# Performance work log

Hardware: AMD Instinct MI355X
Metric: run time of the kernel (lower is better)

Reference implementation:

```python
import jax, jax.numpy as jnp
import numpy as np

DIM = 768
H = 6        # pinned by router mask construction (3 logits -> 6 head gates)
HD = DIM // H  # 128
TAU = 5.0

def setup_inputs() -> dict:
    key = jax.random.key(0)
    ks = jax.random.split(key, 10)
    w = 0.02
    return {
        "x": jax.random.normal(ks[0], (4, 2048, DIM), jnp.float32),
        "latency": jax.random.uniform(ks[1], (1,), jnp.float32),
        "qkv_w": jax.random.normal(ks[2], (3 * DIM, DIM), jnp.float32) * w,
        "qkv_b": jax.random.normal(ks[3], (3 * DIM,), jnp.float32) * w,
        "proj_w": jax.random.normal(ks[4], (DIM, DIM), jnp.float32) * w,
        "proj_b": jax.random.normal(ks[5], (DIM,), jnp.float32) * w,
        "router_w": jax.random.normal(ks[6], (3, 1), jnp.float32),
        "router_b": jax.random.normal(ks[7], (3,), jnp.float32),
        # gumbel noise g = -log(Exp(1)), matching -empty.exponential_().log()
        "g1": -jnp.log(jax.random.exponential(ks[8], (3,), jnp.float32)),
        "g2": -jnp.log(jax.random.exponential(ks[9], (3,), jnp.float32)),
    }

def reference(x, latency, qkv_w, qkv_b, proj_w, proj_b, router_w, router_b, g1, g2):
    # router: Linear(1, 3) on scalar latency -> 3 logits
    logits = router_w @ latency + router_b                      # [3]
    # gumbel-sigmoid, tau=5, hard=True with straight-through estimator
    y_soft = jax.nn.sigmoid((logits + g1 - g2) / TAU)           # [3]
    y_hard = (y_soft > 0.5).astype(y_soft.dtype)
    mask3 = y_hard - jax.lax.stop_gradient(y_soft) + y_soft     # [3]
    # first logit gates 4 heads, remaining two gate one head each -> 6 heads
    mask6 = jnp.concatenate([mask3[:1], mask3[:1], mask3[:1], mask3])  # [6]
    maskC = jnp.repeat(mask6, HD)                               # [DIM]

    B, N, C = x.shape
    qkv = jnp.einsum('bnc,oc->bno', x, qkv_w) + qkv_b           # [B,N,3*DIM]
    qkv = qkv.reshape(B, N, 3, H, HD)
    q, k, v = qkv[:, :, 0], qkv[:, :, 1], qkv[:, :, 2]          # [B,N,H,HD]

    scale = HD ** -0.5
    attn = jax.nn.softmax(jnp.einsum('bqhd,bkhd->bhqk', q * scale, k), axis=-1)
    out = jnp.einsum('bhqk,bkhd->bqhd', attn, v).reshape(B, N, C)

    out = out * maskC                                            # gate heads/channels
    return jnp.einsum('bnc,oc->bno', out, proj_w) + proj_b
```

## Files before the change

### kernel.cpp

```cpp
#include <hip/hip_runtime.h>
#include <cstdint>

#define DIM_ 768
#define H_ 6
#define HD_ 128
#define NB_ 4
#define SEQ_ 2048
#define TOK_ (NB_*SEQ_)
#define OUT3_ (3*DIM_)
#define L2E 1.4426950408889634f

typedef __bf16 bf16;
typedef __bf16 bf16x4 __attribute__((ext_vector_type(4)));
typedef __bf16 bf16x8 __attribute__((ext_vector_type(8)));
typedef float f32x4 __attribute__((ext_vector_type(4)));
typedef float f32x16 __attribute__((ext_vector_type(16)));
typedef unsigned int u32;
typedef u32 u32x4 __attribute__((ext_vector_type(4)));

__device__ __forceinline__ void gload16(const void* g, void* lds) {
  __builtin_amdgcn_global_load_lds((const __attribute__((address_space(1))) void*)g,
                                   (__attribute__((address_space(3))) void*)lds,
                                   16, 0, 0);
}

__global__ void convert_kernel(const float* __restrict__ in, bf16* __restrict__ out, int n) {
  int i = (blockIdx.x * 256 + threadIdx.x) * 4;
  if (i >= n) return;
  float4 v = *reinterpret_cast<const float4*>(in + i);
  bf16x4 o = { (bf16)v.x, (bf16)v.y, (bf16)v.z, (bf16)v.w };
  *reinterpret_cast<bf16x4*>(out + i) = o;
}

__global__ void mask_kernel(const float* __restrict__ latency,
                            const float* __restrict__ rw,
                            const float* __restrict__ rb,
                            const float* __restrict__ g1,
                            const float* __restrict__ g2,
                            float* __restrict__ mask6) {
  int i = threadIdx.x;
  if (i < 6) {
    int j = (i < 4) ? 0 : (i - 3);
    float logit = rw[j] * latency[0] + rb[j];
    float z = (logit + g1[j] - g2[j]) / 5.0f;
    float ys = 1.0f / (1.0f + expf(-z));
    float yh = ys > 0.5f ? 1.0f : 0.0f;
    mask6[i] = (yh - ys) + ys;
  }
}


__global__ __launch_bounds__(256)
void qkv_gemm(const bf16* __restrict__ A, const bf16* __restrict__ W,
              const float* __restrict__ bias,
              bf16* __restrict__ q, bf16* __restrict__ k, bf16* __restrict__ vt) {
  __shared__ bf16 As[128 * 32];
  __shared__ bf16 Bs[128 * 32];
  __shared__ bf16 FragS[8192];
  const int tid = threadIdx.x;
  const int l = tid & 63, w = tid >> 6;
  const int lr = l & 15, lg = l >> 4;
  const int wm = w >> 1, wn = w & 1;
  const int tm = blockIdx.y * 128;
  const int on = blockIdx.x * 128;

  f32x4 acc[4][4];
#pragma unroll
  for (int i = 0; i < 4; ++i)
#pragma unroll
    for (int j = 0; j < 4; ++j) acc[i][j] = f32x4{0.f, 0.f, 0.f, 0.f};

  for (int k0 = 0; k0 < DIM_; k0 += 32) {
    __syncthreads();
#pragma unroll
    for (int u = 0; u < 2; ++u) {
      int row = w * 32 + u * 16 + (l >> 2);
      int cb = l & 3;
      gload16(A + (size_t)(tm + row) * DIM_ + k0 + cb * 8, As + (w * 32 + u * 16) * 32);
      gload16(W + (size_t)(on + row) * DIM_ + k0 + cb * 8, Bs + (w * 32 + u * 16) * 32);
    }
    __syncthreads();
    bf16x8 af[4], bfr[4];
#pragma unroll
    for (int i = 0; i < 4; ++i)
      af[i] = *reinterpret_cast<const bf16x8*>(As + (wm * 64 + i * 16 + lr) * 32 + lg * 8);
#pragma unroll
    for (int j = 0; j < 4; ++j)
      bfr[j] = *reinterpret_cast<const bf16x8*>(Bs + (wn * 64 + j * 16 + lr) * 32 + lg * 8);
#pragma unroll
    for (int i = 0; i < 4; ++i)
#pragma unroll
      for (int j = 0; j < 4; ++j)
        acc[i][j] = __builtin_amdgcn_mfma_f32_16x16x32_bf16(af[i], bfr[j], acc[i][j], 0, 0, 0);
  }

  if (on < 2 * DIM_) {
    const int s = on / DIM_;
    const float scale = 0.08838834764831845f * L2E;
    const int n0 = tm & 2047;
    const int bb = tm >> 11;
    const int hh = (on - s * DIM_) >> 7;
    const int bhh = bb * H_ + hh;
    bf16* dstbase = (s == 0) ? q : k;
    for (int pass = 0; pass < 2; ++pass) {
      __syncthreads();
      if (wm == pass) {
#pragma unroll
        for (int i = 0; i < 4; ++i) {
#pragma unroll
          for (int j = 0; j < 4; ++j) {
            int dd = wn * 64 + j * 16 + lr;
            int kc = dd >> 4, hi8 = (dd >> 3) & 1, e = dd & 7;
            float bia = bias[on + dd];
#pragma unroll
            for (int r = 0; r < 4; ++r) {
              int nl = i * 16 + lg * 4 + r;
              float val = acc[i][j][r] + bia;
              if (s == 0) val *= scale;
              FragS[(((nl >> 5) * 8 + kc) << 9) + ((hi8 * 32 + (nl & 31)) << 3) + e] = (bf16)val;
            }
          }
        }
      }
      __syncthreads();
      size_t base = ((size_t)bhh * 64 + (n0 >> 5) + pass * 2) * 4096;
#pragma unroll
      for (int r8 = 0; r8 < 4; ++r8) {
        bf16x8 v8 = *reinterpret_cast<const bf16x8*>(FragS + r8 * 2048 + tid * 8);
        *reinterpret_cast<bf16x8*>(dstbase + base + r8 * 2048 + tid * 8) = v8;
      }
    }
  } else {
    const int hh = (on - 2 * DIM_) >> 7;
    const int bb = tm >> 11, n0 = tm & 2047;
    const int bhh = bb * H_ + hh;
    bf16(*Ts)[136] = reinterpret_cast<bf16(*)[136]>(As);
    for (int wc = 0; wc < 2; ++wc) {
#pragma unroll
      for (int j = 0; j < 4; ++j) {
        __syncthreads();
        if (wn == wc) {
          float bia = bias[on + wc * 64 + j * 16 + lr];
#pragma unroll
          for (int i = 0; i < 4; ++i) {
            bf16x4 pk;
#pragma unroll
            for (int r = 0; r < 4; ++r) pk[r] = (bf16)(acc[i][j][r] + bia);
            *reinterpret_cast<bf16x4*>(&Ts[lr][wm * 64 + i * 16 + lg * 4]) = pk;
          }
        }
        __syncthreads();
        int row = tid >> 4;
        int c8 = (tid & 15) * 8;
        bf16x8 v8 = *reinterpret_cast<const bf16x8*>(&Ts[row][c8]);
        int d = wc * 64 + j * 16 + row;
        int n = n0 + c8;
        size_t idx = (((((size_t)bhh * 32 + (n >> 6)) * 4 + ((n >> 4) & 3)) * 4 + (d >> 5)) << 9) +
                     ((((n >> 3) & 1) * 32 + (d & 31)) << 3);
        *reinterpret_cast<bf16x8*>(vt + idx) = v8;
      }
    }
  }
}

__global__ __launch_bounds__(256)
void proj_gemm(const bf16* __restrict__ A, const bf16* __restrict__ W,
               const float* __restrict__ bias, float* __restrict__ out) {
  __shared__ bf16 As[128 * 32];
  __shared__ bf16 Bs[128 * 32];
  const int tid = threadIdx.x;
  const int l = tid & 63, w = tid >> 6;
  const int lr = l & 15, lg = l >> 4;
  const int wm = w >> 1, wn = w & 1;
  const int tm = blockIdx.y * 128;
  const int on = blockIdx.x * 128;

  f32x4 acc[4][4];
#pragma unroll
  for (int i = 0; i < 4; ++i)
#pragma unroll
    for (int j = 0; j < 4; ++j) acc[i][j] = f32x4{0.f, 0.f, 0.f, 0.f};

  for (int k0 = 0; k0 < DIM_; k0 += 32) {
    __syncthreads();
#pragma unroll
    for (int u = 0; u < 2; ++u) {
      int row = w * 32 + u * 16 + (l >> 2);
      int cb = l & 3;
      gload16(A + (size_t)(tm + row) * DIM_ + k0 + cb * 8, As + (w * 32 + u * 16) * 32);
      gload16(W + (size_t)(on + row) * DIM_ + k0 + cb * 8, Bs + (w * 32 + u * 16) * 32);
    }
    __syncthreads();
    bf16x8 af[4], bfr[4];
#pragma unroll
    for (int i = 0; i < 4; ++i)
      af[i] = *reinterpret_cast<const bf16x8*>(As + (wm * 64 + i * 16 + lr) * 32 + lg * 8);
#pragma unroll
    for (int j = 0; j < 4; ++j)
      bfr[j] = *reinterpret_cast<const bf16x8*>(Bs + (wn * 64 + j * 16 + lr) * 32 + lg * 8);
#pragma unroll
    for (int i = 0; i < 4; ++i)
#pragma unroll
      for (int j = 0; j < 4; ++j)
        acc[i][j] = __builtin_amdgcn_mfma_f32_16x16x32_bf16(af[i], bfr[j], acc[i][j], 0, 0, 0);
  }

#pragma unroll
  for (int i = 0; i < 4; ++i) {
#pragma unroll
    for (int j = 0; j < 4; ++j) {
      int o = on + wn * 64 + j * 16 + lr;
      float bia = bias[o];
#pragma unroll
      for (int r = 0; r < 4; ++r) {
        int t = tm + wm * 64 + i * 16 + lg * 4 + r;
        out[(size_t)t * DIM_ + o] = acc[i][j][r] + bia;
      }
    }
  }
}

__global__ __launch_bounds__(256)
void attn_kernel(const bf16* __restrict__ qf_g, const bf16* __restrict__ kf_g,
                 const bf16* __restrict__ vf_g, const float* __restrict__ mask6,
                 bf16* __restrict__ ab) {
  __shared__ char smem[33280];

  const int tid = threadIdx.x;
  const int l = tid & 63;
  const int w = tid >> 6;
  const int half = w >> 1, qw = w & 1;
  const int kl = l & 31, hi = l >> 5;
  const int bid = blockIdx.x;
  const int bh = bid % 24;
  const int qt2 = bid / 24;
  const int h = bh % H_;
  const int b = bh / H_;
  const int q0 = qt2 * 64 + qw * 32;
  const int loff = l * 8;
  const float hm = mask6[h];

  if (hm == 0.0f) {
    bf16x8 z = __builtin_bit_cast(bf16x8, u32x4{0u, 0u, 0u, 0u});
    int row = tid >> 2, c0 = (tid & 3) * 32;
    bf16* dst = ab + ((size_t)b * SEQ_ + qt2 * 64 + row) * DIM_ + h * HD_ + c0;
#pragma unroll
    for (int u = 0; u < 4; ++u)
      *reinterpret_cast<bf16x8*>(dst + u * 8) = z;
    return;
  }

  bf16* KSh = (bf16*)(smem + half * 8192);
  bf16* VSh = (bf16*)(smem + 16384 + half * 8192);
  float* MLm = (float*)(smem + 32768);
  float* MLl = MLm + 64;

  const bf16* qq = qf_g + (((size_t)bh * 64 + qt2 * 2 + qw) * 8) * 512;
  const bf16* kq = kf_g + (size_t)bh * 262144;
  const bf16* vq = vf_g + (size_t)bh * 262144;

  bf16x8 qf[8];
#pragma unroll
  for (int kc = 0; kc < 8; ++kc)
    qf[kc] = *reinterpret_cast<const bf16x8*>(qq + kc * 512 + loff);

  f32x16 oacc[4];
#pragma unroll
  for (int df = 0; df < 4; ++df)
#pragma unroll
    for (int r = 0; r < 16; ++r) oacc[df][r] = 0.f;
  float m_lane = -3.0e38f;
  float lsum = 0.f;

  for (int it = 0; it < 32; ++it) {
    int jj = half * 32 + it;
#pragma unroll
    for (int u = 0; u < 4; ++u) {
      int c = qw * 4 + u;
      gload16(kq + (size_t)jj * 4096 + c * 512 + loff, KSh + c * 512);
      gload16(vq + (size_t)jj * 4096 + c * 512 + loff, VSh + c * 512);
    }
    __syncthreads();

    f32x16 sacc;
#pragma unroll
    for (int r = 0; r < 16; ++r) sacc[r] = 0.f;
    __builtin_amdgcn_s_setprio(1);
#pragma unroll
    for (int kc = 0; kc < 8; ++kc) {
      bf16x8 kfr = *reinterpret_cast<const bf16x8*>(KSh + kc * 512 + loff);
      sacc = __builtin_amdgcn_mfma_f32_32x32x16_bf16(kfr, qf[kc], sacc, 0, 0, 0);
    }
    __builtin_amdgcn_s_setprio(0);

    float t = sacc[0];
#pragma unroll
    for (int r = 1; r < 16; ++r) t = fmaxf(t, sacc[r]);
    t = fmaxf(t, __shfl_xor(t, 32));
    bool need = t > m_lane + 8.0f;
    if (__ballot(need) != 0ull) {
      float nm = fmaxf(m_lane, t);
      float c = exp2f(m_lane - nm);
      m_lane = nm;
      lsum *= c;
#pragma unroll
      for (int r = 0; r < 16; ++r) {
        float cr = __shfl(c, (r & 3) + 8 * (r >> 2) + 4 * hi);
#pragma unroll
        for (int df = 0; df < 4; ++df) oacc[df][r] *= cr;
      }
    }

    u32 pp[8];
#pragma unroll
    for (int m = 0; m < 8; ++m) {
      float e0 = exp2f(sacc[2 * m] - m_lane);
      float e1 = exp2f(sacc[2 * m + 1] - m_lane);
      lsum += e0 + e1;
      union { u32 u; bf16 hh2[2]; } pk;
      pk.hh2[0] = (bf16)e0; pk.hh2[1] = (bf16)e1;
      pp[m] = pk.u;
    }

    u32x4 afv[2];
#pragma unroll
    for (int ks = 0; ks < 2; ++ks) {
#pragma unroll
      for (int i = 0; i < 2; ++i) {
        u32 a = pp[4 * ks + i];
        u32 b2 = pp[4 * ks + 2 + i];
        asm volatile("v_permlane32_swap_b32 %0, %1" : "+v"(a), "+v"(b2));
        afv[ks][i] = a;
        afv[ks][2 + i] = b2;
      }
    }

    __builtin_amdgcn_s_setprio(1);
#pragma unroll
    for (int ks = 0; ks < 2; ++ks) {
      bf16x8 pa = __builtin_bit_cast(bf16x8, afv[ks]);
#pragma unroll
      for (int df = 0; df < 4; ++df) {
        bf16x8 vfr = *reinterpret_cast<const bf16x8*>(VSh + (ks * 4 + df) * 512 + loff);
        oacc[df] = __builtin_amdgcn_mfma_f32_32x32x16_bf16(pa, vfr, oacc[df], 0, 0, 0);
      }
    }
    __builtin_amdgcn_s_setprio(0);

    __syncthreads();
  }

  float lt = lsum + __shfl_xor(lsum, 32);

  float* OM = (float*)smem;
  if (half == 1) {
#pragma unroll
    for (int r = 0; r < 16; ++r) {
      int qloc = (r & 3) + 8 * (r >> 2) + 4 * hi;
#pragma unroll
      for (int df = 0; df < 4; ++df)
        OM[qw * 4096 + qloc * 128 + df * 32 + kl] = oacc[df][r];
    }
    MLm[qw * 32 + kl] = m_lane;
    MLl[qw * 32 + kl] = lt;
  }
  __syncthreads();
  if (half == 1) return;

  float m1 = MLm[qw * 32 + kl];
  float l1 = MLl[qw * 32 + kl];
  float M = fmaxf(m_lane, m1);
  float a0 = exp2f(m_lane - M), a1 = exp2f(m1 - M);
  float L = lt * a0 + l1 * a1;
  float s0 = a0 * hm / L, s1 = a1 * hm / L;

#pragma unroll
  for (int r = 0; r < 16; ++r) {
    int qloc = (r & 3) + 8 * (r >> 2) + 4 * hi;
    float r0 = __shfl(s0, qloc);
    float r1 = __shfl(s1, qloc);
    int n = q0 + qloc;
#pragma unroll
    for (int df = 0; df < 4; ++df) {
      int d = df * 32 + kl;
      float o1 = OM[qw * 4096 + qloc * 128 + df * 32 + kl];
      ab[((size_t)b * SEQ_ + n) * DIM_ + h * HD_ + d] =
          (bf16)(oacc[df][r] * r0 + o1 * r1);
    }
  }
}

extern "C" void kernel_launch(void* const* d_in, const int* in_sizes, int n_in,
                              void* d_out, int out_size, void* d_ws, size_t ws_size,
                              hipStream_t stream) {
  const float* x        = (const float*)d_in[0];
  const float* latency  = (const float*)d_in[1];
  const float* qkv_w    = (const float*)d_in[2];
  const float* qkv_b    = (const float*)d_in[3];
  const float* proj_w   = (const float*)d_in[4];
  const float* proj_b   = (const float*)d_in[5];
  const float* router_w = (const float*)d_in[6];
  const float* router_b = (const float*)d_in[7];
  const float* g1       = (const float*)d_in[8];
  const float* g2       = (const float*)d_in[9];
  float* out = (float*)d_out;

  const size_t N_X  = (size_t)TOK_ * DIM_;
  const size_t N_WQ = (size_t)OUT3_ * DIM_;
  const size_t N_WP = (size_t)DIM_ * DIM_;
  const size_t N_P  = (size_t)NB_ * H_ * SEQ_ * HD_;

  float* maskp = (float*)d_ws;
  bf16* xb  = (bf16*)((char*)d_ws + 256);
  bf16* wqb = xb + N_X;
  bf16* wpb = wqb + N_WQ;
  bf16* qbf = wpb + N_WP;
  bf16* kbf = qbf + N_P;
  bf16* vtb = kbf + N_P;
  bf16* abf = vtb + N_P;

  size_t need = 256 + 2 * (N_X + N_WQ + N_WP + 4 * N_P);
  if (ws_size < need) return;

  convert_kernel<<<(int)(N_X / 1024), 256, 0, stream>>>(x, xb, (int)N_X);
  convert_kernel<<<(int)(N_WQ / 1024), 256, 0, stream>>>(qkv_w, wqb, (int)N_WQ);
  convert_kernel<<<(int)(N_WP / 1024), 256, 0, stream>>>(proj_w, wpb, (int)N_WP);
  mask_kernel<<<1, 64, 0, stream>>>(latency, router_w, router_b, g1, g2, maskp);

  qkv_gemm<<<dim3(OUT3_ / 128, TOK_ / 128), 256, 0, stream>>>(xb, wqb, qkv_b, qbf, kbf, vtb);
  attn_kernel<<<dim3(24 * (SEQ_ / 64)), 256, 0, stream>>>(qbf, kbf, vtb, maskp, abf);
  proj_gemm<<<dim3(DIM_ / 128, TOK_ / 128), 256, 0, stream>>>(abf, wpb, proj_b, out);
}
```

Measured before the change: 195.6 us.

## Fuse x bf16 conversion into QKV GEMM and drop LDS staging in attention

The QKV GEMM now reads fp32 x directly, converts each tile to bf16 in registers and stores it into shared memory. This removes the separate x conversion kernel and its bf16 workspace round trip. The attention kernel shrinks to 128 threads handling 32 queries per block. Each wave loads K/V fragments straight from global memory instead of staging them through LDS with per-iteration barriers, so its two waves split the key range. This removes barriers and LDS traffic, but K/V no longer get shared between query waves, which raises L2/global traffic and exposes load latency with no explicit prefetch.

New measurement: 208.4 us. 1.07x slower.

```diff
diff --git a/kernel.cpp b/kernel.cpp
--- a/kernel.cpp
+++ b/kernel.cpp
@@ -51,7 +51,7 @@
 
 
 __global__ __launch_bounds__(256)
-void qkv_gemm(const bf16* __restrict__ A, const bf16* __restrict__ W,
+void qkv_gemm(const float* __restrict__ X, const bf16* __restrict__ W,
               const float* __restrict__ bias,
               bf16* __restrict__ q, bf16* __restrict__ k, bf16* __restrict__ vt) {
   __shared__ bf16 As[128 * 32];
@@ -76,7 +76,12 @@
     for (int u = 0; u < 2; ++u) {
       int row = w * 32 + u * 16 + (l >> 2);
       int cb = l & 3;
-      gload16(A + (size_t)(tm + row) * DIM_ + k0 + cb * 8, As + (w * 32 + u * 16) * 32);
+      const float* ap = X + (size_t)(tm + row) * DIM_ + k0 + cb * 8;
+      float4 f0 = *reinterpret_cast<const float4*>(ap);
+      float4 f1 = *reinterpret_cast<const float4*>(ap + 4);
+      bf16x8 a8 = { (bf16)f0.x, (bf16)f0.y, (bf16)f0.z, (bf16)f0.w,
+                    (bf16)f1.x, (bf16)f1.y, (bf16)f1.z, (bf16)f1.w };
+      *reinterpret_cast<bf16x8*>(As + (w * 32 + u * 16) * 32 + l * 8) = a8;
       gload16(W + (size_t)(on + row) * DIM_ + k0 + cb * 8, Bs + (w * 32 + u * 16) * 32);
     }
     __syncthreads();
@@ -220,44 +225,42 @@
   }
 }
 
-__global__ __launch_bounds__(256)
+__global__ __launch_bounds__(128, 3)
 void attn_kernel(const bf16* __restrict__ qf_g, const bf16* __restrict__ kf_g,
                  const bf16* __restrict__ vf_g, const float* __restrict__ mask6,
                  bf16* __restrict__ ab) {
-  __shared__ char smem[33280];
+  __shared__ char smem[16640];
 
   const int tid = threadIdx.x;
   const int l = tid & 63;
   const int w = tid >> 6;
-  const int half = w >> 1, qw = w & 1;
   const int kl = l & 31, hi = l >> 5;
   const int bid = blockIdx.x;
   const int bh = bid % 24;
-  const int qt2 = bid / 24;
+  const int qt = bid / 24;
   const int h = bh % H_;
   const int b = bh / H_;
-  const int q0 = qt2 * 64 + qw * 32;
+  const int q0 = qt * 32;
   const int loff = l * 8;
   const float hm = mask6[h];
 
   if (hm == 0.0f) {
     bf16x8 z = __builtin_bit_cast(bf16x8, u32x4{0u, 0u, 0u, 0u});
     int row = tid >> 2, c0 = (tid & 3) * 32;
-    bf16* dst = ab + ((size_t)b * SEQ_ + qt2 * 64 + row) * DIM_ + h * HD_ + c0;
+    bf16* dst = ab + ((size_t)b * SEQ_ + q0 + row) * DIM_ + h * HD_ + c0;
 #pragma unroll
     for (int u = 0; u < 4; ++u)
       *reinterpret_cast<bf16x8*>(dst + u * 8) = z;
     return;
   }
 
-  bf16* KSh = (bf16*)(smem + half * 8192);
-  bf16* VSh = (bf16*)(smem + 16384 + half * 8192);
-  float* MLm = (float*)(smem + 32768);
-  float* MLl = MLm + 64;
-
-  const bf16* qq = qf_g + (((size_t)bh * 64 + qt2 * 2 + qw) * 8) * 512;
-  const bf16* kq = kf_g + (size_t)bh * 262144;
-  const bf16* vq = vf_g + (size_t)bh * 262144;
+  float* OM  = (float*)smem;
+  float* MLm = (float*)(smem + 16384);
+  float* MLl = MLm + 32;
+
+  const bf16* qq = qf_g + (((size_t)bh * 64 + qt) * 8) * 512;
+  const bf16* kq = kf_g + (size_t)bh * 262144 + (size_t)w * 32 * 4096;
+  const bf16* vq = vf_g + (size_t)bh * 262144 + (size_t)w * 32 * 4096;
 
   bf16x8 qf[8];
 #pragma unroll
@@ -272,15 +275,9 @@
   float m_lane = -3.0e38f;
   float lsum = 0.f;
 
-  for (int it = 0; it < 32; ++it) {
-    int jj = half * 32 + it;
-#pragma unroll
-    for (int u = 0; u < 4; ++u) {
-      int c = qw * 4 + u;
-      gload16(kq + (size_t)jj * 4096 + c * 512 + loff, KSh + c * 512);
-      gload16(vq + (size_t)jj * 4096 + c * 512 + loff, VSh + c * 512);
-    }
-    __syncthreads();
+  for (int jj = 0; jj < 32; ++jj) {
+    const bf16* kb = kq + (size_t)jj * 4096;
+    const bf16* vb = vq + (size_t)jj * 4096;
 
     f32x16 sacc;
 #pragma unroll
@@ -288,7 +285,7 @@
     __builtin_amdgcn_s_setprio(1);
 #pragma unroll
     for (int kc = 0; kc < 8; ++kc) {
-      bf16x8 kfr = *reinterpret_cast<const bf16x8*>(KSh + kc * 512 + loff);
+      bf16x8 kfr = *reinterpret_cast<const bf16x8*>(kb + kc * 512 + loff);
       sacc = __builtin_amdgcn_mfma_f32_32x32x16_bf16(kfr, qf[kc], sacc, 0, 0, 0);
     }
     __builtin_amdgcn_s_setprio(0);
@@ -341,34 +338,31 @@
       bf16x8 pa = __builtin_bit_cast(bf16x8, afv[ks]);
 #pragma unroll
       for (int df = 0; df < 4; ++df) {
-        bf16x8 vfr = *reinterpret_cast<const bf16x8*>(VSh + (ks * 4 + df) * 512 + loff);
+        bf16x8 vfr = *reinterpret_cast<const bf16x8*>(vb + (ks * 4 + df) * 512 + loff);
         oacc[df] = __builtin_amdgcn_mfma_f32_32x32x16_bf16(pa, vfr, oacc[df], 0, 0, 0);
       }
     }
     __builtin_amdgcn_s_setprio(0);
-
-    __syncthreads();
   }
 
   float lt = lsum + __shfl_xor(lsum, 32);
 
-  float* OM = (float*)smem;
-  if (half == 1) {
+  if (w == 1) {
 #pragma unroll
     for (int r = 0; r < 16; ++r) {
       int qloc = (r & 3) + 8 * (r >> 2) + 4 * hi;
 #pragma unroll
       for (int df = 0; df < 4; ++df)
-        OM[qw * 4096 + qloc * 128 + df * 32 + kl] = oacc[df][r];
-    }
-    MLm[qw * 32 + kl] = m_lane;
-    MLl[qw * 32 + kl] = lt;
+        OM[qloc * 128 + df * 32 + kl] = oacc[df][r];
+    }
+    MLm[kl] = m_lane;
+    MLl[kl] = lt;
   }
   __syncthreads();
-  if (half == 1) return;
-
-  float m1 = MLm[qw * 32 + kl];
-  float l1 = MLl[qw * 32 + kl];
+  if (w == 1) return;
+
+  float m1 = MLm[kl];
+  float l1 = MLl[kl];
   float M = fmaxf(m_lane, m1);
   float a0 = exp2f(m_lane - M), a1 = exp2f(m1 - M);
   float L = lt * a0 + l1 * a1;
@@ -383,7 +377,7 @@
 #pragma unroll
     for (int df = 0; df < 4; ++df) {
       int d = df * 32 + kl;
-      float o1 = OM[qw * 4096 + qloc * 128 + df * 32 + kl];
+      float o1 = OM[qloc * 128 + df * 32 + kl];
       ab[((size_t)b * SEQ_ + n) * DIM_ + h * HD_ + d] =
           (bf16)(oacc[df][r] * r0 + o1 * r1);
     }
@@ -405,29 +399,26 @@
   const float* g2       = (const float*)d_in[9];
   float* out = (float*)d_out;
 
-  const size_t N_X  = (size_t)TOK_ * DIM_;
   const size_t N_WQ = (size_t)OUT3_ * DIM_;
   const size_t N_WP = (size_t)DIM_ * DIM_;
   const size_t N_P  = (size_t)NB_ * H_ * SEQ_ * HD_;
 
   float* maskp = (float*)d_ws;
-  bf16* xb  = (bf16*)((char*)d_ws + 256);
-  bf16* wqb = xb + N_X;
+  bf16* wqb = (bf16*)((char*)d_ws + 256);
   bf16* wpb = wqb + N_WQ;
   bf16* qbf = wpb + N_WP;
   bf16* kbf = qbf + N_P;
   bf16* vtb = kbf + N_P;
   bf16* abf = vtb + N_P;
 
-  size_t need = 256 + 2 * (N_X + N_WQ + N_WP + 4 * N_P);
+  size_t need = 256 + 2 * (N_WQ + N_WP + 4 * N_P);
   if (ws_size < need) return;
 
-  convert_kernel<<<(int)(N_X / 1024), 256, 0, stream>>>(x, xb, (int)N_X);
   convert_kernel<<<(int)(N_WQ / 1024), 256, 0, stream>>>(qkv_w, wqb, (int)N_WQ);
   convert_kernel<<<(int)(N_WP / 1024), 256, 0, stream>>>(proj_w, wpb, (int)N_WP);
   mask_kernel<<<1, 64, 0, stream>>>(latency, router_w, router_b, g1, g2, maskp);
 
-  qkv_gemm<<<dim3(OUT3_ / 128, TOK_ / 128), 256, 0, stream>>>(xb, wqb, qkv_b, qbf, kbf, vtb);
-  attn_kernel<<<dim3(24 * (SEQ_ / 64)), 256, 0, stream>>>(qbf, kbf, vtb, maskp, abf);
+  qkv_gemm<<<dim3(OUT3_ / 128, TOK_ / 128), 256, 0, stream>>>(x, wqb, qkv_b, qbf, kbf, vtb);
+  attn_kernel<<<dim3(24 * (SEQ_ / 32)), 128, 0, stream>>>(qbf, kbf, vtb, maskp, abf);
   proj_gemm<<<dim3(DIM_ / 128, TOK_ / 128), 256, 0, stream>>>(abf, wpb, proj_b, out);
 }
```
